# Kernel tuning notes

Measured on AMD Instinct MI355X. Metric: run time of the kernel, lower is better.

The kernel has to match this reference:

```python
import jax, jax.numpy as jnp
import numpy as np

B, S, D = 4, 2048, 1024
H = 8
HD = D // H          # head_dim = 128
SCALE = 1.0 / np.sqrt(HD)


def setup_inputs() -> dict:
    key = jax.random.key(0)
    ks = jax.random.split(key, 9)
    def lin_w(k):
        return jax.random.normal(k, (D, D), dtype=jnp.float32) * (1.0 / np.sqrt(D))
    return {
        "hidden_states": jax.random.normal(ks[0], (B, S, D), dtype=jnp.float32),
        "Wq": lin_w(ks[1]), "bq": jax.random.normal(ks[2], (D,), dtype=jnp.float32) * 0.02,
        "Wk": lin_w(ks[3]), "bk": jax.random.normal(ks[4], (D,), dtype=jnp.float32) * 0.02,
        "Wv": lin_w(ks[5]), "bv": jax.random.normal(ks[6], (D,), dtype=jnp.float32) * 0.02,
        "Wo": lin_w(ks[7]), "bo": jax.random.normal(ks[8], (D,), dtype=jnp.float32) * 0.02,
    }


def reference(hidden_states, Wq, bq, Wk, bk, Wv, bv, Wo, bo):
    b, s, _ = hidden_states.shape
    # Linear projections (torch nn.Linear: x @ W.T + b; here W stored as (D, D) acting as W.T)
    Q = hidden_states @ Wq + bq
    K = hidden_states @ Wk + bk
    V = hidden_states @ Wv + bv
    # (b, h, s, hd)
    Q = Q.reshape(b, s, H, HD).transpose(0, 2, 1, 3)
    K = K.reshape(b, s, H, HD).transpose(0, 2, 1, 3)
    V = V.reshape(b, s, H, HD).transpose(0, 2, 1, 3)
    # Quaternion inner product sum_quat Re(k* \otimes q) == plain dot product over head_dim:
    # conjugation negates (x,y,z) and the Hamilton real part w1w2 - x1x2 - y1y2 - z1z2
    # re-negates them, yielding wK wQ + xK xQ + yK yQ + zK zQ per quaternion.
    scores = jnp.einsum("bhqd,bhkd->bhqk", Q, K) * SCALE
    attn = jax.nn.softmax(scores, axis=-1)
    out = jnp.einsum("bhqk,bhkd->bhqd", attn, V)
    out = out.transpose(0, 2, 1, 3).reshape(b, s, D)
    return out @ Wo + bo
```

## Files before the change

kernel.cpp:

```cpp
#include <hip/hip_runtime.h>

typedef _Float16 h8 __attribute__((ext_vector_type(8)));
typedef float fx4 __attribute__((ext_vector_type(4)));

#define D_ 1024
#define S_ 2048
#define H_ 8
#define HD_ 128
static constexpr float SCALE = 0.0883883476483184405f;
static constexpr float LOG2E = 1.44269504088896f;
static constexpr float M0C = 5.0f * 1.44269504088896f;

typedef __attribute__((address_space(3))) void lds_void_t;
typedef __attribute__((address_space(1))) void g_void_t;

__device__ __forceinline__ void gl_lds16(const void* g, void* l) {
  __builtin_amdgcn_global_load_lds((const g_void_t*)(uintptr_t)g,
                                   (lds_void_t*)(uintptr_t)l, 16, 0, 0);
}

__device__ __forceinline__ float fast_exp2(float x) {
#if __has_builtin(__builtin_amdgcn_exp2f)
  return __builtin_amdgcn_exp2f(x);
#else
  return __expf(x * 0.6931471805599453f);
#endif
}

__global__ void cast_f16_kernel(const float* __restrict__ x, _Float16* __restrict__ y, int n8) {
  int i = blockIdx.x * blockDim.x + threadIdx.x;
  if (i >= n8) return;
  float4 v0 = ((const float4*)x)[2 * i];
  float4 v1 = ((const float4*)x)[2 * i + 1];
  h8 o = { (_Float16)v0.x, (_Float16)v0.y, (_Float16)v0.z, (_Float16)v0.w,
           (_Float16)v1.x, (_Float16)v1.y, (_Float16)v1.z, (_Float16)v1.w };
  ((h8*)y)[i] = o;
}

__global__ void transpose_cast_w(const float* __restrict__ W, _Float16* __restrict__ Wt) {
  __shared__ float tile[32][33];
  int bx = blockIdx.x * 32, by = blockIdx.y * 32;
  int tx = threadIdx.x, ty = threadIdx.y;
  for (int i = ty; i < 32; i += 8)
    tile[i][tx] = W[(by + i) * D_ + bx + tx];
  __syncthreads();
  for (int i = ty; i < 32; i += 8)
    Wt[(bx + i) * D_ + by + tx] = (_Float16)tile[tx][i];
}

__global__ void transpose_v(const _Float16* __restrict__ Vh, _Float16* __restrict__ Vt) {
  __shared__ _Float16 tile[32][33];
  int s0 = blockIdx.x * 32, d0 = blockIdx.y * 32;
  int bh = blockIdx.z;
  int b = bh >> 3, h = bh & 7;
  int tx = threadIdx.x, ty = threadIdx.y;
  for (int i = ty; i < 32; i += 8)
    tile[i][tx] = Vh[(b * S_ + s0 + i) * D_ + h * HD_ + d0 + tx];
  __syncthreads();
  for (int i = ty; i < 32; i += 8)
    Vt[(bh * HD_ + d0 + i) * S_ + s0 + tx] = tile[tx][i];
}

template <typename OutT>
__device__ __forceinline__ void gemm_body(const _Float16* __restrict__ A,
                                          const _Float16* __restrict__ Bt,
                                          const float* __restrict__ bias,
                                          OutT* __restrict__ C, int m0, int n0) {
  constexpr int K = 1024, N = 1024;
  __shared__ __align__(16) _Float16 As[128 * 64];
  __shared__ __align__(16) _Float16 Bs[128 * 64];
  int tid = threadIdx.x;
  int lane = tid & 63, w = tid >> 6;
  int wr = w >> 1, wc = w & 1;
  int l16 = lane & 15, quad = lane >> 4;
  fx4 acc[4][4] = {};
  for (int k0 = 0; k0 < K; k0 += 64) {
#pragma unroll
    for (int it = 0; it < 4; ++it) {
      int s = it * 256 + tid;
      int row = s >> 3, gc = (s & 7) ^ (row & 7);
      gl_lds16(&A[(m0 + row) * K + k0 + gc * 8], &As[s * 8]);
      gl_lds16(&Bt[(n0 + row) * K + k0 + gc * 8], &Bs[s * 8]);
    }
    __syncthreads();
#pragma unroll
    for (int kk = 0; kk < 2; ++kk) {
      h8 a[4], b[4];
#pragma unroll
      for (int i = 0; i < 4; ++i) {
        int row = wr * 64 + i * 16 + l16;
        a[i] = *(const h8*)&As[(row * 8 + ((kk * 4 + quad) ^ (row & 7))) * 8];
      }
#pragma unroll
      for (int j = 0; j < 4; ++j) {
        int row = wc * 64 + j * 16 + l16;
        b[j] = *(const h8*)&Bs[(row * 8 + ((kk * 4 + quad) ^ (row & 7))) * 8];
      }
#pragma unroll
      for (int i = 0; i < 4; ++i)
#pragma unroll
        for (int j = 0; j < 4; ++j)
          acc[i][j] = __builtin_amdgcn_mfma_f32_16x16x32_f16(a[i], b[j], acc[i][j], 0, 0, 0);
    }
    __syncthreads();
  }
#pragma unroll
  for (int i = 0; i < 4; ++i) {
    int row = m0 + wr * 64 + i * 16 + quad * 4;
#pragma unroll
    for (int j = 0; j < 4; ++j) {
      int col = n0 + wc * 64 + j * 16 + l16;
      float bv_ = bias[col];
#pragma unroll
      for (int r = 0; r < 4; ++r)
        C[(row + r) * N + col] = (OutT)(acc[i][j][r] + bv_);
    }
  }
}

__global__ __launch_bounds__(256) void gemm_qkv(const _Float16* __restrict__ A,
                                                const _Float16* __restrict__ Wt,
                                                const float* __restrict__ bq,
                                                const float* __restrict__ bk,
                                                const float* __restrict__ bv,
                                                _Float16* __restrict__ QKV) {
  int z = blockIdx.z;
  const float* bias = (z == 0) ? bq : ((z == 1) ? bk : bv);
  gemm_body<_Float16>(A, Wt + z * (D_ * D_), bias, QKV + z * (S_ * 4 * D_),
                      blockIdx.y * 128, blockIdx.x * 128);
}

__global__ __launch_bounds__(256) void gemm_out(const _Float16* __restrict__ A,
                                                const _Float16* __restrict__ Wt,
                                                const float* __restrict__ bias,
                                                float* __restrict__ C) {
  gemm_body<float>(A, Wt, bias, C, blockIdx.y * 128, blockIdx.x * 128);
}

__global__ __launch_bounds__(256, 2) void attn_kernel(const _Float16* __restrict__ Qh,
                                                      const _Float16* __restrict__ Kh,
                                                      const _Float16* __restrict__ Vt,
                                                      _Float16* __restrict__ Oh) {
  __shared__ __align__(16) _Float16 Ks[2][64 * 128];
  __shared__ __align__(16) _Float16 Vs[128 * 64];
  __shared__ __align__(16) _Float16 Ps[4 * 32 * 64];
  const int tid = threadIdx.x;
  const int lane = tid & 63, w = tid >> 6;
  const int l16 = lane & 15, quad = lane >> 4;

  const int lin = blockIdx.y * gridDim.x + blockIdx.x;
  const int xcd = lin & 7, idx = lin >> 3;
  const int bh = (idx >> 4) * 8 + xcd;
  const int qblk = idx & 15;
  const int b = bh >> 3, h = bh & 7;
  const int q0 = qblk * 128 + w * 32;

  const _Float16* Qp = Qh + (size_t)(b * S_ + q0) * D_ + h * HD_;
  const _Float16* Kp = Kh + (size_t)(b * S_) * D_ + h * HD_;
  const _Float16* Vp = Vt + (size_t)bh * HD_ * S_;
  _Float16* Pw = &Ps[w * 32 * 64];

  int kOff[4], vOff[4], ldsOff[4];
#pragma unroll
  for (int it = 0; it < 4; ++it) {
    int s = it * 256 + tid;
    int rowK = s >> 4, gcK = (s & 15) ^ (rowK & 7);
    kOff[it] = rowK * D_ + gcK * 8;
    int rowV = s >> 3, gcV = (s & 7) ^ (rowV & 7);
    vOff[it] = rowV * S_ + gcV * 8;
    ldsOff[it] = s * 8;
  }

  h8 aq[2][4];
#pragma unroll
  for (int mi = 0; mi < 2; ++mi)
#pragma unroll
    for (int kk = 0; kk < 4; ++kk) {
      h8 v = *(const h8*)&Qp[(mi * 16 + l16) * D_ + kk * 32 + quad * 8];
      aq[mi][kk] = v * (_Float16)(SCALE * LOG2E);
    }

  h8 ones_b;
  {
    _Float16 o1 = (l16 == 0) ? (_Float16)1.0f : (_Float16)0.0f;
    ones_b = (h8){o1, o1, o1, o1, o1, o1, o1, o1};
  }

  fx4 o[2][8] = {};
  fx4 lacc[2] = {};

#pragma unroll
  for (int it = 0; it < 4; ++it)
    gl_lds16(Kp + kOff[it], &Ks[0][ldsOff[it]]);

  for (int t = 0; t < 32; ++t) {
    const int kt = t * 64;
    const int cb = t & 1;
    __syncthreads();

    if (t + 1 < 32) {
#pragma unroll
      for (int it = 0; it < 4; ++it)
        gl_lds16(Kp + (kt + 64) * D_ + kOff[it], &Ks[cb ^ 1][ldsOff[it]]);
    }
#pragma unroll
    for (int it = 0; it < 4; ++it)
      gl_lds16(Vp + kt + vOff[it], &Vs[ldsOff[it]]);

    fx4 s_[2][4];
#pragma unroll
    for (int mi = 0; mi < 2; ++mi)
#pragma unroll
      for (int j = 0; j < 4; ++j) s_[mi][j] = (fx4){-M0C, -M0C, -M0C, -M0C};
#pragma unroll
    for (int j = 0; j < 4; ++j) {
      int row = j * 16 + l16;
      h8 bk[4];
#pragma unroll
      for (int kk = 0; kk < 4; ++kk)
        bk[kk] = *(const h8*)&Ks[cb][(row * 16 + ((kk * 4 + quad) ^ (row & 7))) * 8];
#pragma unroll
      for (int kk = 0; kk < 4; ++kk) {
        s_[0][j] = __builtin_amdgcn_mfma_f32_16x16x32_f16(aq[0][kk], bk[kk], s_[0][j], 0, 0, 0);
        s_[1][j] = __builtin_amdgcn_mfma_f32_16x16x32_f16(aq[1][kk], bk[kk], s_[1][j], 0, 0, 0);
      }
    }

#pragma unroll
    for (int mi = 0; mi < 2; ++mi)
#pragma unroll
      for (int r = 0; r < 4; ++r) {
        int row = mi * 16 + quad * 4 + r;
#pragma unroll
        for (int j = 0; j < 4; ++j) {
          float p = fast_exp2(s_[mi][j][r]);
          int c = j * 2 + (l16 >> 3);
          Pw[row * 64 + ((c + row) & 7) * 8 + (l16 & 7)] = (_Float16)p;
        }
      }

    __syncthreads();

    h8 ap[2][2];
#pragma unroll
    for (int mi = 0; mi < 2; ++mi)
#pragma unroll
      for (int kk = 0; kk < 2; ++kk) {
        int row = mi * 16 + l16;
        ap[mi][kk] = *(const h8*)&Pw[row * 64 + (((kk * 4 + quad) + row) & 7) * 8];
      }

#pragma unroll
    for (int jd = 0; jd < 8; ++jd) {
      int row = jd * 16 + l16;
#pragma unroll
      for (int kk = 0; kk < 2; ++kk) {
        h8 bv = *(const h8*)&Vs[(row * 8 + ((kk * 4 + quad) ^ (row & 7))) * 8];
        o[0][jd] = __builtin_amdgcn_mfma_f32_16x16x32_f16(ap[0][kk], bv, o[0][jd], 0, 0, 0);
        o[1][jd] = __builtin_amdgcn_mfma_f32_16x16x32_f16(ap[1][kk], bv, o[1][jd], 0, 0, 0);
      }
    }
#pragma unroll
    for (int kk = 0; kk < 2; ++kk) {
      lacc[0] = __builtin_amdgcn_mfma_f32_16x16x32_f16(ap[0][kk], ones_b, lacc[0], 0, 0, 0);
      lacc[1] = __builtin_amdgcn_mfma_f32_16x16x32_f16(ap[1][kk], ones_b, lacc[1], 0, 0, 0);
    }
  }

#pragma unroll
  for (int mi = 0; mi < 2; ++mi)
#pragma unroll
    for (int r = 0; r < 4; ++r) {
      float lsum = __shfl(lacc[mi][r], lane & 48);
      float inv = 1.0f / lsum;
      int row = q0 + mi * 16 + quad * 4 + r;
      _Float16* op = Oh + (size_t)(b * S_ + row) * D_ + h * HD_;
#pragma unroll
      for (int jd = 0; jd < 8; ++jd)
        op[jd * 16 + l16] = (_Float16)(o[mi][jd][r] * inv);
    }
}

extern "C" void kernel_launch(void* const* d_in, const int* in_sizes, int n_in,
                              void* d_out, int out_size, void* d_ws, size_t ws_size,
                              hipStream_t stream) {
  const float* hs = (const float*)d_in[0];
  const float* Wq = (const float*)d_in[1];
  const float* bq = (const float*)d_in[2];
  const float* Wk = (const float*)d_in[3];
  const float* bk = (const float*)d_in[4];
  const float* Wv = (const float*)d_in[5];
  const float* bv = (const float*)d_in[6];
  const float* Wo = (const float*)d_in[7];
  const float* bo = (const float*)d_in[8];
  float* out = (float*)d_out;

  const int MD = S_ * 4 * D_;
  const int WD = D_ * D_;
  _Float16* ws = (_Float16*)d_ws;
  _Float16* hs_h = ws;
  _Float16* WtQ = hs_h + MD;
  _Float16* WtO = WtQ + 3 * WD;
  _Float16* QKVh = WtO + WD;
  _Float16* Vt = QKVh + 3 * MD;
  _Float16* Oh = Vt + MD;

  dim3 tb(32, 8);
  cast_f16_kernel<<<MD / 8 / 256, 256, 0, stream>>>(hs, hs_h, MD / 8);
  transpose_cast_w<<<dim3(32, 32), tb, 0, stream>>>(Wq, WtQ);
  transpose_cast_w<<<dim3(32, 32), tb, 0, stream>>>(Wk, WtQ + WD);
  transpose_cast_w<<<dim3(32, 32), tb, 0, stream>>>(Wv, WtQ + 2 * WD);
  transpose_cast_w<<<dim3(32, 32), tb, 0, stream>>>(Wo, WtO);

  gemm_qkv<<<dim3(8, 64, 3), 256, 0, stream>>>(hs_h, WtQ, bq, bk, bv, QKVh);
  transpose_v<<<dim3(S_ / 32, HD_ / 32, 32), tb, 0, stream>>>(QKVh + 2 * MD, Vt);
  attn_kernel<<<dim3(S_ / 128, 32), 256, 0, stream>>>(QKVh, QKVh + MD, Vt, Oh);
  gemm_out<<<dim3(8, 64), 256, 0, stream>>>(Oh, WtO, bo, out);
}
```

Before: 312.1 us.

## Software-pipeline attention PV with next QK tile and batch weight transposes

The attention loop now double-buffers the V tile in LDS and defers each tile's P·V and row-sum MFMAs to the next iteration, where they run after that iteration's QK^T MFMAs. A final epilogue handles the last tile. This removes the mid-iteration barrier, so exp/softmax work and V loads can overlap with matrix-core work. It also merges the four weight transpose-cast launches into one 3D-grid launch. In exchange, LDS use per block rises, which may limit occupancy at the requested two blocks per CU.

```diff
diff --git a/kernel.cpp b/kernel.cpp
--- a/kernel.cpp
+++ b/kernel.cpp
@@ -37,15 +37,19 @@
   ((h8*)y)[i] = o;
 }
 
-__global__ void transpose_cast_w(const float* __restrict__ W, _Float16* __restrict__ Wt) {
+__global__ void transpose_cast_w4(const float* __restrict__ W0, const float* __restrict__ W1,
+                                  const float* __restrict__ W2, const float* __restrict__ W3,
+                                  _Float16* __restrict__ Wt) {
   __shared__ float tile[32][33];
+  const float* W = (blockIdx.z == 0) ? W0 : (blockIdx.z == 1) ? W1 : (blockIdx.z == 2) ? W2 : W3;
+  _Float16* dst = Wt + (size_t)blockIdx.z * D_ * D_;
   int bx = blockIdx.x * 32, by = blockIdx.y * 32;
   int tx = threadIdx.x, ty = threadIdx.y;
   for (int i = ty; i < 32; i += 8)
     tile[i][tx] = W[(by + i) * D_ + bx + tx];
   __syncthreads();
   for (int i = ty; i < 32; i += 8)
-    Wt[(bx + i) * D_ + by + tx] = (_Float16)tile[tx][i];
+    dst[(bx + i) * D_ + by + tx] = (_Float16)tile[tx][i];
 }
 
 __global__ void transpose_v(const _Float16* __restrict__ Vh, _Float16* __restrict__ Vt) {
@@ -142,7 +146,7 @@
                                                       const _Float16* __restrict__ Vt,
                                                       _Float16* __restrict__ Oh) {
   __shared__ __align__(16) _Float16 Ks[2][64 * 128];
-  __shared__ __align__(16) _Float16 Vs[128 * 64];
+  __shared__ __align__(16) _Float16 Vs[2][128 * 64];
   __shared__ __align__(16) _Float16 Ps[4 * 32 * 64];
   const int tid = threadIdx.x;
   const int lane = tid & 63, w = tid >> 6;
@@ -198,14 +202,14 @@
     const int cb = t & 1;
     __syncthreads();
 
-    if (t + 1 < 32) {
+    if (t < 31) {
 #pragma unroll
       for (int it = 0; it < 4; ++it)
         gl_lds16(Kp + (kt + 64) * D_ + kOff[it], &Ks[cb ^ 1][ldsOff[it]]);
     }
 #pragma unroll
     for (int it = 0; it < 4; ++it)
-      gl_lds16(Vp + kt + vOff[it], &Vs[ldsOff[it]]);
+      gl_lds16(Vp + kt + vOff[it], &Vs[cb][ldsOff[it]]);
 
     fx4 s_[2][4];
 #pragma unroll
@@ -223,6 +227,32 @@
       for (int kk = 0; kk < 4; ++kk) {
         s_[0][j] = __builtin_amdgcn_mfma_f32_16x16x32_f16(aq[0][kk], bk[kk], s_[0][j], 0, 0, 0);
         s_[1][j] = __builtin_amdgcn_mfma_f32_16x16x32_f16(aq[1][kk], bk[kk], s_[1][j], 0, 0, 0);
+      }
+    }
+
+    if (t > 0) {
+      h8 ap[2][2];
+#pragma unroll
+      for (int mi = 0; mi < 2; ++mi)
+#pragma unroll
+        for (int kk = 0; kk < 2; ++kk) {
+          int row = mi * 16 + l16;
+          ap[mi][kk] = *(const h8*)&Pw[row * 64 + (((kk * 4 + quad) + row) & 7) * 8];
+        }
+#pragma unroll
+      for (int jd = 0; jd < 8; ++jd) {
+        int row = jd * 16 + l16;
+#pragma unroll
+        for (int kk = 0; kk < 2; ++kk) {
+          h8 bv = *(const h8*)&Vs[cb ^ 1][(row * 8 + ((kk * 4 + quad) ^ (row & 7))) * 8];
+          o[0][jd] = __builtin_amdgcn_mfma_f32_16x16x32_f16(ap[0][kk], bv, o[0][jd], 0, 0, 0);
+          o[1][jd] = __builtin_amdgcn_mfma_f32_16x16x32_f16(ap[1][kk], bv, o[1][jd], 0, 0, 0);
+        }
+      }
+#pragma unroll
+      for (int kk = 0; kk < 2; ++kk) {
+        lacc[0] = __builtin_amdgcn_mfma_f32_16x16x32_f16(ap[0][kk], ones_b, lacc[0], 0, 0, 0);
+        lacc[1] = __builtin_amdgcn_mfma_f32_16x16x32_f16(ap[1][kk], ones_b, lacc[1], 0, 0, 0);
       }
     }
 
@@ -238,9 +268,11 @@
           Pw[row * 64 + ((c + row) & 7) * 8 + (l16 & 7)] = (_Float16)p;
         }
       }
-
-    __syncthreads();
-
+  }
+
+  __syncthreads();
+
+  {
     h8 ap[2][2];
 #pragma unroll
     for (int mi = 0; mi < 2; ++mi)
@@ -249,13 +281,12 @@
         int row = mi * 16 + l16;
         ap[mi][kk] = *(const h8*)&Pw[row * 64 + (((kk * 4 + quad) + row) & 7) * 8];
       }
-
 #pragma unroll
     for (int jd = 0; jd < 8; ++jd) {
       int row = jd * 16 + l16;
 #pragma unroll
       for (int kk = 0; kk < 2; ++kk) {
-        h8 bv = *(const h8*)&Vs[(row * 8 + ((kk * 4 + quad) ^ (row & 7))) * 8];
+        h8 bv = *(const h8*)&Vs[1][(row * 8 + ((kk * 4 + quad) ^ (row & 7))) * 8];
         o[0][jd] = __builtin_amdgcn_mfma_f32_16x16x32_f16(ap[0][kk], bv, o[0][jd], 0, 0, 0);
         o[1][jd] = __builtin_amdgcn_mfma_f32_16x16x32_f16(ap[1][kk], bv, o[1][jd], 0, 0, 0);
       }
@@ -307,10 +338,7 @@
 
   dim3 tb(32, 8);
   cast_f16_kernel<<<MD / 8 / 256, 256, 0, stream>>>(hs, hs_h, MD / 8);
-  transpose_cast_w<<<dim3(32, 32), tb, 0, stream>>>(Wq, WtQ);
-  transpose_cast_w<<<dim3(32, 32), tb, 0, stream>>>(Wk, WtQ + WD);
-  transpose_cast_w<<<dim3(32, 32), tb, 0, stream>>>(Wv, WtQ + 2 * WD);
-  transpose_cast_w<<<dim3(32, 32), tb, 0, stream>>>(Wo, WtO);
+  transpose_cast_w4<<<dim3(32, 32, 4), tb, 0, stream>>>(Wq, Wk, Wv, Wo, WtQ);
 
   gemm_qkv<<<dim3(8, 64, 3), 256, 0, stream>>>(hs_h, WtQ, bq, bk, bv, QKVh);
   transpose_v<<<dim3(S_ / 32, HD_ / 32, 32), tb, 0, stream>>>(QKVh + 2 * MD, Vt);
```

Result: faster. 297.4 us (-4.7%).
